# Kernel tuning notes

Hardware: AMD Instinct MI355X
Metric: run time of the kernel (lower is better)

## Reference

```python
import jax, jax.numpy as jnp
import numpy as np

B, TIN, E, TOUT, NMEL = 32, 512, 576, 400, 80
PRE, ARNN, DRNN, ADIM, NF, KS = 256, 1024, 1024, 128, 32, 31


def setup_inputs() -> dict:
    key = jax.random.key(0)
    ks = jax.random.split(key, 24)
    r = lambda i, sh, s=0.02: jax.random.normal(ks[i], sh, dtype=jnp.float32) * s
    return {
        'memory': jax.random.normal(ks[0], (B, TIN, E), dtype=jnp.float32) * 0.5,
        'decoder_inputs': jax.random.normal(ks[1], (B, TOUT, NMEL), dtype=jnp.float32) * 0.5,
        'prenet_W1': r(2, (PRE, NMEL)),
        'prenet_W2': r(3, (PRE, PRE)),
        'att_Wih': r(4, (4 * ARNN, PRE + E)),
        'att_Whh': r(5, (4 * ARNN, ARNN)),
        'att_bih': r(6, (4 * ARNN,)),
        'att_bhh': r(7, (4 * ARNN,)),
        'qW': r(8, (ADIM, ARNN)),
        'memW': r(9, (ADIM, E)),
        'convW': r(10, (NF, 2, KS)),
        'convb': r(11, (NF,)),
        'locW': r(12, (ADIM, NF)),
        'vW': r(13, (ADIM,)),
        'dec_Wih': r(14, (4 * DRNN, ARNN + E)),
        'dec_Whh': r(15, (4 * DRNN, DRNN)),
        'dec_bih': r(16, (4 * DRNN,)),
        'dec_bhh': r(17, (4 * DRNN,)),
        'projW': r(18, (NMEL, DRNN + E)),
        'projb': r(19, (NMEL,)),
        'gateW': r(20, (1, DRNN + E)),
        'gateb': r(21, (1,)),
        'memory_lengths': jnp.clip(jax.random.randint(ks[22], (B,), 1, TIN + 1), 16, TIN),
    }


def _lstm(x, h, c, Wih, Whh, bih, bhh):
    g = x @ Wih.T + bih + h @ Whh.T + bhh
    i, f, gg, o = jnp.split(g, 4, axis=-1)  # torch LSTMCell gate order i,f,g,o
    c = jax.nn.sigmoid(f) * c + jax.nn.sigmoid(i) * jnp.tanh(gg)
    h = jax.nn.sigmoid(o) * jnp.tanh(c)
    return h, c


def _forward(memory, decoder_inputs, prenet_W1, prenet_W2, att_Wih, att_Whh, att_bih,
             att_bhh, qW, memW, convW, convb, locW, vW, dec_Wih, dec_Whh, dec_bih,
             dec_bhh, projW, projb, gateW, gateb, memory_lengths):
    b, tin, e = memory.shape
    # go frame + teacher forcing inputs -> prenet (dropout off in deterministic eval)
    go = jnp.zeros((b, 1, NMEL), dtype=memory.dtype)
    di = jnp.concatenate([go, decoder_inputs], axis=1)          # [B, T+1, NMEL]
    x = jax.nn.relu(di @ prenet_W1.T)
    x = jax.nn.relu(x @ prenet_W2.T)                            # [B, T+1, PRE]
    xs = jnp.swapaxes(x, 0, 1)[:-1]                             # [T, B, PRE]
    pmem = memory @ memW.T                                      # [B, TIN, ADIM]
    invalid = jnp.arange(tin)[None, :] >= memory_lengths[:, None]
    pad = KS // 2

    init = (jnp.zeros((b, ARNN)), jnp.zeros((b, ARNN)),
            jnp.zeros((b, DRNN)), jnp.zeros((b, DRNN)),
            jnp.zeros((b, tin)), jnp.zeros((b, tin)),
            jnp.zeros((b, e)))

    def step(carry, xt):
        ah, ac, dh, dc, aw, awc, ctx = carry
        ci = jnp.concatenate([xt, ctx], axis=-1)
        ah, ac = _lstm(ci, ah, ac, att_Wih, att_Whh, att_bih, att_bhh)
        ah = ac  # faithful to source: dropout(attention_cell) overwrites hidden (identity in eval)
        wc = jnp.stack([aw, awc], axis=1)                       # [B, 2, TIN]
        loc = jax.lax.conv_general_dilated(
            wc, convW, (1,), [(pad, pad)],
            dimension_numbers=('NCH', 'OIH', 'NCH')) + convb[None, :, None]
        loc = jnp.swapaxes(loc, 1, 2) @ locW.T                  # [B, TIN, ADIM]
        q = (ah @ qW.T)[:, None, :]                             # [B, 1, ADIM]
        en = jnp.tanh(q + pmem + loc) @ vW                      # [B, TIN]
        en = jnp.where(invalid, -jnp.inf, en)
        aw = jax.nn.softmax(en, axis=1)
        ctx = jnp.einsum('bt,bte->be', aw, memory)
        awc = awc + aw
        d_in = jnp.concatenate([ah, ctx], axis=-1)
        dh, dc = _lstm(d_in, dh, dc, dec_Wih, dec_Whh, dec_bih, dec_bhh)
        dhc = jnp.concatenate([dh, ctx], axis=-1)
        mel = dhc @ projW.T + projb                             # [B, NMEL]
        gate = (dhc @ gateW.T + gateb)[:, 0]                    # [B]
        return (ah, ac, dh, dc, aw, awc, ctx), (mel, gate, aw)

    _, (mels, gates, aligns) = jax.lax.scan(step, init, xs)
    mel_out = jnp.swapaxes(jnp.swapaxes(mels, 0, 1), 1, 2)      # [B, NMEL, T]
    gate_out = jnp.swapaxes(gates, 0, 1)                        # [B, T]
    align_out = jnp.swapaxes(aligns, 0, 1)                      # [B, T, TIN]
    return mel_out, gate_out, align_out


def reference(memory, decoder_inputs, prenet_W1, prenet_W2, att_Wih, att_Whh, att_bih,
              att_bhh, qW, memW, convW, convb, locW, vW, dec_Wih, dec_Whh, dec_bih,
              dec_bhh, projW, projb, gateW, gateb, memory_lengths):
    return _forward(memory, decoder_inputs, prenet_W1, prenet_W2, att_Wih, att_Whh,
                    att_bih, att_bhh, qW, memW, convW, convb, locW, vW, dec_Wih,
                    dec_Whh, dec_bih, dec_bhh, projW, projb, gateW, gateb,
                    memory_lengths)
```

## Files before the change

### kernel.cpp

```cpp
#include <hip/hip_runtime.h>
#include <stdint.h>


#define NB  32
#define TI  512
#define ED  576
#define TO  400
#define NM  80
#define PR  256
#define AR  1024
#define DR  1024
#define AD  128
#define NFl 32
#define KSz 31
#define KA  1856
#define KD  2624
#define NKT_A 58
#define NKT_D 82
#define FPAD 32
#define MF_OFF (257*FPAD)

#define SCR_CWB 3584
#define SCR_ACC 4608
#define SCR_DCC 4736
#define SCR_SQ  4864
#define LDS_WA_BYTES (NKT_A*512*2)
#define LDS_WD_BYTES (NKT_D*512*2)
#define LDS_SCR_FLOATS 4992
#define LDS_TOTAL (LDS_WA_BYTES + LDS_WD_BYTES + LDS_SCR_FLOATS*4)

typedef __attribute__((ext_vector_type(8))) short bf8_t;
typedef __attribute__((ext_vector_type(4))) float f4_t;
typedef __attribute__((ext_vector_type(2))) float f2_t;
typedef unsigned long long ull;

__device__ __forceinline__ short f2bf(float f){
  union { float f; unsigned u; } v; v.f = f;
  unsigned r = v.u + 0x7fffu + ((v.u >> 16) & 1u);
  return (short)(r >> 16);
}
__device__ __forceinline__ float bf2f(short s){
  union { unsigned u; float f; } v; v.u = ((unsigned)(unsigned short)s) << 16; return v.f;
}
__device__ __forceinline__ float sigm(float x){ return 1.f / (1.f + __expf(-x)); }

__device__ __forceinline__ f4_t MFMA(bf8_t a, bf8_t b, f4_t c){
  return __builtin_amdgcn_mfma_f32_16x16x32_bf16(a, b, c, 0, 0, 0);
}

__device__ __forceinline__ float cld(const float* p){
  return __hip_atomic_load(p, __ATOMIC_RELAXED, __HIP_MEMORY_SCOPE_AGENT);
}
__device__ __forceinline__ void cst(float* p, float v){
  __hip_atomic_store(p, v, __ATOMIC_RELAXED, __HIP_MEMORY_SCOPE_AGENT);
}
__device__ __forceinline__ ull cld8(const void* p){
  return __hip_atomic_load((const ull*)p, __ATOMIC_RELAXED, __HIP_MEMORY_SCOPE_AGENT);
}
__device__ __forceinline__ void cst8(void* p, ull v){
  __hip_atomic_store((ull*)p, v, __ATOMIC_RELAXED, __HIP_MEMORY_SCOPE_AGENT);
}
__device__ __forceinline__ bf8_t cld_bf8(const short* p){
  union { bf8_t v; ull q[2]; } u;
  u.q[0] = cld8(p); u.q[1] = cld8(p + 4);
  return u.v;
}
__device__ __forceinline__ void cst_bf8(short* p, bf8_t v){
  union { bf8_t v; ull q[2]; } u; u.v = v;
  cst8(p, u.q[0]); cst8(p + 4, u.q[1]);
}

__device__ __forceinline__ bf8_t packrow(const float* p){
  f4_t a = *(const f4_t*)p;
  f4_t b = *(const f4_t*)(p + 4);
  bf8_t r;
  r[0]=f2bf(a[0]); r[1]=f2bf(a[1]); r[2]=f2bf(a[2]); r[3]=f2bf(a[3]);
  r[4]=f2bf(b[0]); r[5]=f2bf(b[1]); r[6]=f2bf(b[2]); r[7]=f2bf(b[3]);
  return r;
}
__device__ __forceinline__ bf8_t packrow_coh(const float* p){
  union { ull q; float f[2]; } u0, u1, u2, u3;
  u0.q = cld8(p); u1.q = cld8(p + 2); u2.q = cld8(p + 4); u3.q = cld8(p + 6);
  bf8_t r;
  r[0]=f2bf(u0.f[0]); r[1]=f2bf(u0.f[1]);
  r[2]=f2bf(u1.f[0]); r[3]=f2bf(u1.f[1]);
  r[4]=f2bf(u2.f[0]); r[5]=f2bf(u2.f[1]);
  r[6]=f2bf(u3.f[0]); r[7]=f2bf(u3.f[1]);
  return r;
}

struct Par {
  const float *X2;
  const short *PMEMH;
  const short *WA, *WD, *WQ, *WLOC, *MEMBT, *PJW;
  const float *BSA, *BSD;
  const float *convW, *convb, *vW;
  const float *projb, *gateb;
  const int *mlen;
  float *AC, *DH, *CTX, *AW, *AWC, *EN, *QP;
  short *ABA, *ABD;
  float *out_mel, *out_gate, *out_align;
  unsigned *FLAGS;
};

__device__ __forceinline__ const float* aptr_att(const Par& p, int rp, int t, int b, int k){
  if (k < PR)      return p.X2 + ((size_t)t*NB + b)*PR + k;
  if (k < PR+ED)   return p.CTX + (size_t)rp*NB*ED + b*ED + (k - PR);
  return p.AC + (size_t)b*AR + (k - PR - ED);
}

__device__ __forceinline__ void loadD(const Par& p, int cpar, int ks, int lane,
                                      bf8_t& a0, bf8_t& a1){
  if (ks >= 32 && ks < 50){
    const int kb = ks*32 + ((lane >> 4) << 3);
    const float* c0 = p.CTX + (size_t)cpar*NB*ED + (size_t)(lane & 15)*ED + (kb - AR);
    const float* c1 = p.CTX + (size_t)cpar*NB*ED + (size_t)(16 + (lane & 15))*ED + (kb - AR);
    a0 = packrow_coh(c0);
    a1 = packrow_coh(c1);
  } else {
    a0 = cld_bf8(p.ABD + ((size_t)(0*NKT_D + ks)*64 + lane)*8);
    a1 = cld_bf8(p.ABD + ((size_t)(1*NKT_D + ks)*64 + lane)*8);
  }
}

__device__ __forceinline__ void gbar(unsigned* flags, unsigned tgt){
  __syncthreads();
  if (threadIdx.x == 0)
    __hip_atomic_store(&flags[blockIdx.x*FPAD], tgt, __ATOMIC_RELAXED, __HIP_MEMORY_SCOPE_AGENT);
  if (blockIdx.x == 0){
    if (threadIdx.x < 256){
      while (__hip_atomic_load(&flags[threadIdx.x*FPAD], __ATOMIC_RELAXED, __HIP_MEMORY_SCOPE_AGENT) < tgt) {}
    }
    __syncthreads();
    if (threadIdx.x == 0)
      __hip_atomic_store(&flags[256*FPAD], tgt, __ATOMIC_RELAXED, __HIP_MEMORY_SCOPE_AGENT);
  }
  if (threadIdx.x == 0){
    while (__hip_atomic_load(&flags[256*FPAD], __ATOMIC_RELAXED, __HIP_MEMORY_SCOPE_AGENT) < tgt) {}
  }
  __syncthreads();
}

__device__ __forceinline__ void sibbar(unsigned* mf, int bid, int tid, unsigned tgt){
  __syncthreads();
  if (tid == 0)
    __hip_atomic_store(&mf[bid*FPAD], tgt, __ATOMIC_RELAXED, __HIP_MEMORY_SCOPE_AGENT);
  const int g = (bid >> 3) << 3;
  if (tid < 8){
    while (__hip_atomic_load(&mf[(g + tid)*FPAD], __ATOMIC_RELAXED, __HIP_MEMORY_SCOPE_AGENT) < tgt) {}
  }
  __syncthreads();
}

__device__ __forceinline__ void reduce8(float* scr, f4_t& a0, f4_t& a1, int lane, int wv){
  if (wv > 0){
    float* slot = scr + (size_t)((wv - 1)*64 + lane)*8;
    *(f4_t*)slot       = a0;
    *(f4_t*)(slot + 4) = a1;
  }
  __syncthreads();
  if (wv == 0){
    #pragma unroll
    for (int w = 0; w < 7; ++w){
      const float* s2 = scr + (size_t)(w*64 + lane)*8;
      a0 += *(const f4_t*)s2;
      a1 += *(const f4_t*)(s2 + 4);
    }
  }
  __syncthreads();
}

__device__ __forceinline__ void dec_gates_cell(const Par& p, const short* sWD, float* scr,
                                               float* sDCc, int cpar, int bid,
                                               int lane, int wv, int tid){
  f4_t acc0 = (f4_t){0.f,0.f,0.f,0.f}, acc1 = (f4_t){0.f,0.f,0.f,0.f};
  {
    bf8_t A0[6], A1[6];
    #pragma unroll
    for (int i = 0; i < 6; ++i) loadD(p, cpar, wv + i*8, lane, A0[i], A1[i]);
    #pragma unroll
    for (int i = 0; i < 6; ++i){
      const bf8_t bw = *((const bf8_t*)sWD + (wv + i*8)*64 + lane);
      acc0 = MFMA(A0[i], bw, acc0);
      acc1 = MFMA(A1[i], bw, acc1);
    }
  }
  {
    bf8_t A0[5], A1[5];
    #pragma unroll
    for (int i = 0; i < 5; ++i){
      const int ks = wv + (i + 6)*8;
      if (ks < NKT_D) loadD(p, cpar, ks, lane, A0[i], A1[i]);
    }
    #pragma unroll
    for (int i = 0; i < 5; ++i){
      const int ks = wv + (i + 6)*8;
      if (ks < NKT_D){
        const bf8_t bw = *((const bf8_t*)sWD + ks*64 + lane);
        acc0 = MFMA(A0[i], bw, acc0);
        acc1 = MFMA(A1[i], bw, acc1);
      }
    }
  }
  reduce8(scr, acc0, acc1, lane, wv);
  float* sG = scr;
  if (wv == 0){
    const int col = lane & 15, rb2 = (lane >> 4) << 2;
    const int jp = (col & 3)*1024 + bid*4 + (col >> 2);
    const float bs = p.BSD[jp];
    #pragma unroll
    for (int r = 0; r < 4; ++r){
      sG[(rb2 + r)*16 + col]      = acc0[r] + bs;
      sG[(16 + rb2 + r)*16 + col] = acc1[r] + bs;
    }
  }
  __syncthreads();
  if (tid < 128){
    const int b = tid >> 2, ul = tid & 3;
    const float gi = sG[b*16 + ul*4 + 0];
    const float gf = sG[b*16 + ul*4 + 1];
    const float gg = sG[b*16 + ul*4 + 2];
    const float go = sG[b*16 + ul*4 + 3];
    const float c  = sigm(gf) * sDCc[tid] + sigm(gi) * tanhf(gg);
    sDCc[tid] = c;
    cst(&p.DH[(size_t)b*DR + bid*4 + ul], sigm(go) * tanhf(c));
  }
  __syncthreads();
}

__device__ void dec_proj(const Par& p, int b, int tprev, int tid, float* sIN){
  const float* ctxg = p.CTX + (size_t)(tprev & 1)*NB*ED + b*ED;
  float h0  = cld(&p.DH[(size_t)b*DR + tid]);
  float h1  = cld(&p.DH[(size_t)b*DR + 512 + tid]);
  float cx0 = cld(ctxg + tid);
  float cx1 = (tid < ED - 512) ? cld(ctxg + 512 + tid) : 0.f;
  sIN[tid] = h0; sIN[512 + tid] = h1;
  sIN[1024 + tid] = cx0;
  if (tid < ED - 512) sIN[1536 + tid] = cx1;
  if (tid < 448) sIN[1600 + tid] = 0.f;
  __syncthreads();
  const int lane = tid & 63, wv = tid >> 6;
  for (int o = wv; o < 81; o += 8){
    const short* wr = p.PJW + (size_t)o*2048 + lane*8;
    float s = 0.f;
    #pragma unroll
    for (int j = 0; j < 4; ++j){
      const bf8_t w8 = *(const bf8_t*)(wr + j*512);
      const float* v = sIN + j*512 + lane*8;
      s += v[0]*bf2f(w8[0]) + v[1]*bf2f(w8[1]) + v[2]*bf2f(w8[2]) + v[3]*bf2f(w8[3])
         + v[4]*bf2f(w8[4]) + v[5]*bf2f(w8[5]) + v[6]*bf2f(w8[6]) + v[7]*bf2f(w8[7]);
    }
    #pragma unroll
    for (int d = 32; d > 0; d >>= 1) s += __shfl_down(s, d);
    if (lane == 0){
      if (o < 80) p.out_mel[((size_t)b*NM + o)*TO + tprev] = s + p.projb[o];
      else        p.out_gate[(size_t)b*TO + tprev] = s + p.gateb[0];
    }
  }
  __syncthreads();
}

__global__ __launch_bounds__(512) void k_loop(Par p){
  const int bid = blockIdx.x, tid = threadIdx.x;
  const int lane = tid & 63, wv = tid >> 6;

  extern __shared__ char dsm[];
  short* sWA = (short*)dsm;
  short* sWD = (short*)(dsm + LDS_WA_BYTES);
  float* scr = (float*)(dsm + LDS_WA_BYTES + LDS_WD_BYTES);
  float* sACc = scr + SCR_ACC;
  float* sDCc = scr + SCR_DCC;
  unsigned* mf = p.FLAGS + MF_OFF;

  const int mlenb = p.mlen[bid >> 3];

  {
    if (tid < 128){ sACc[tid] = 0.f; sDCc[tid] = 0.f; }
    const bf8_t* gwa = (const bf8_t*)(p.WA + (size_t)bid*NKT_A*512);
    bf8_t* lwa = (bf8_t*)sWA;
    for (int i = tid; i < NKT_A*64; i += 512) lwa[i] = gwa[i];
    const bf8_t* gwd = (const bf8_t*)(p.WD + (size_t)bid*NKT_D*512);
    bf8_t* lwd = (bf8_t*)sWD;
    for (int i = tid; i < NKT_D*64; i += 512) lwd[i] = gwd[i];
    __syncthreads();
  }

  for (int t = 0; t < TO; ++t){
    const int wp = t & 1, rp = wp ^ 1;
    const unsigned base = (unsigned)(t * 3);

    {
      f4_t acc0 = (f4_t){0.f,0.f,0.f,0.f}, acc1 = (f4_t){0.f,0.f,0.f,0.f};
      bf8_t A0[8], A1[8];
      #pragma unroll
      for (int i = 0; i < 8; ++i){
        const int ks = wv + i*8;
        if (ks < NKT_A){
          if (t == 0 || (ks >= 8 && ks < 26)){
            const int kb = ks*32 + ((lane >> 4) << 3);
            const float* p0 = aptr_att(p, rp, t, lane & 15, kb);
            const float* p1 = aptr_att(p, rp, t, 16 + (lane & 15), kb);
            if (kb < PR){ A0[i] = packrow(p0);     A1[i] = packrow(p1);     }
            else        { A0[i] = packrow_coh(p0); A1[i] = packrow_coh(p1); }
          } else {
            A0[i] = cld_bf8(p.ABA + ((size_t)(0*NKT_A + ks)*64 + lane)*8);
            A1[i] = cld_bf8(p.ABA + ((size_t)(1*NKT_A + ks)*64 + lane)*8);
          }
        }
      }
      #pragma unroll
      for (int i = 0; i < 8; ++i){
        const int ks = wv + i*8;
        if (ks < NKT_A){
          const bf8_t bw = *((const bf8_t*)sWA + ks*64 + lane);
          acc0 = MFMA(A0[i], bw, acc0);
          acc1 = MFMA(A1[i], bw, acc1);
        }
      }
      reduce8(scr, acc0, acc1, lane, wv);
      float* sG = scr;
      if (wv == 0){
        const int col = lane & 15, rb2 = (lane >> 4) << 2;
        const int jp = (col & 3)*1024 + bid*4 + (col >> 2);
        const float bs = p.BSA[jp];
        #pragma unroll
        for (int r = 0; r < 4; ++r){
          sG[(rb2 + r)*16 + col]      = acc0[r] + bs;
          sG[(16 + rb2 + r)*16 + col] = acc1[r] + bs;
        }
      }
      __syncthreads();
      if (tid < 128){
        const int b = tid >> 2, ul = tid & 3;
        const float gi = sG[b*16 + ul*4 + 0];
        const float gf = sG[b*16 + ul*4 + 1];
        const float gg = sG[b*16 + ul*4 + 2];
        const float c  = sigm(gf) * sACc[tid] + sigm(gi) * tanhf(gg);
        sACc[tid] = c;
        cst(&p.AC[(size_t)b*AR + bid*4 + ul], c);
      }
      __syncthreads();
      if (t > 0) dec_gates_cell(p, sWD, scr, sDCc, rp, bid, lane, wv, tid);
      const int b = bid >> 3, tc = bid & 7, t0 = tc*64;
      float* sAWI = scr;
      short* sCwB = (short*)(scr + SCR_CWB);
      for (int i = tid; i < 94; i += 512){
        int g = t0 - 15 + i;
        float a = 0.f, w = 0.f;
        if (g >= 0 && g < TI){
          a = cld(&p.AW [(size_t)rp*NB*TI + b*TI + g]);
          w = cld(&p.AWC[(size_t)rp*NB*TI + b*TI + g]);
        }
        sAWI[2*i] = a; sAWI[2*i + 1] = w;
      }
      __syncthreads();
      {
        const int wvu = __builtin_amdgcn_readfirstlane(wv);
        const int f0 = wvu * 4;
        float ac4[4];
        #pragma unroll
        for (int ff = 0; ff < 4; ++ff) ac4[ff] = p.convb[f0 + ff];
        for (int k = 0; k < KSz; ++k){
          f2_t a2 = *(const f2_t*)&sAWI[2*(lane + k)];
          #pragma unroll
          for (int ff = 0; ff < 4; ++ff){
            ac4[ff] += a2[0] * p.convW[((f0+ff)*2 + 0)*KSz + k]
                     + a2[1] * p.convW[((f0+ff)*2 + 1)*KSz + k];
          }
        }
        #pragma unroll
        for (int ff = 0; ff < 4; ++ff) sCwB[lane*32 + f0 + ff] = f2bf(ac4[ff]);
      }
    }
    gbar(p.FLAGS, base + 1);

    {
      if (bid < 32){
        const int nt = bid >> 2, kc = bid & 3;
        const int kt = kc*8 + wv;
        const int kb = kt*32 + ((lane >> 4) << 3);
        bf8_t a0 = packrow_coh(p.AC + (size_t)(lane & 15)*AR + kb);
        bf8_t a1 = packrow_coh(p.AC + (size_t)(16 + (lane & 15))*AR + kb);
        const bf8_t bw = *(const bf8_t*)(p.WQ + ((size_t)(nt*32 + kt)*64 + lane)*8);
        f4_t q0 = (f4_t){0.f,0.f,0.f,0.f}, q1 = (f4_t){0.f,0.f,0.f,0.f};
        q0 = MFMA(a0, bw, q0);
        q1 = MFMA(a1, bw, q1);
        reduce8(scr, q0, q1, lane, wv);
        if (wv == 0){
          const int col = lane & 15, rb2 = (lane >> 4) << 2;
          float* qp = p.QP + (size_t)kc*NB*AD;
          #pragma unroll
          for (int r = 0; r < 4; ++r){
            cst(&qp[(rb2 + r)*AD + nt*16 + col],      q0[r]);
            cst(&qp[(16 + rb2 + r)*AD + nt*16 + col], q1[r]);
          }
        }
      }
      if (bid >= 224 && t > 0) dec_proj(p, bid - 224, t - 1, tid, scr);
    }
    gbar(p.FLAGS, base + 2);

    {
      float* sQ = scr + SCR_SQ;
      if (tid < 128){
        const int b = bid >> 3;
        sQ[tid] = cld(&p.QP[(size_t)b*AD + tid])
                + cld(&p.QP[(size_t)NB*AD + b*AD + tid])
                + cld(&p.QP[(size_t)2*NB*AD + b*AD + tid])
                + cld(&p.QP[(size_t)3*NB*AD + b*AD + tid]);
      }
      if (wv == 0 && bid < 208){
        const int r = lane & 15, koff = (lane >> 4) << 3;
        if (bid < 80){
          if (t < TO - 1){
            const int m = bid / 40, idx = bid % 40;
            const int ks = (idx < 8) ? idx : idx + 18;
            const int row = m*16 + r;
            const int k = ks*32 + koff;
            bf8_t v = (k < PR)
              ? packrow(p.X2 + ((size_t)(t+1)*NB + row)*PR + k)
              : packrow_coh(p.AC + (size_t)row*AR + (k - PR - ED));
            cst_bf8(p.ABA + ((size_t)(m*NKT_A + ks)*64 + lane)*8, v);
          }
        } else {
          const int j2 = bid - 80;
          const int m = j2 / 64, idx = j2 % 64;
          const int ks = (idx < 32) ? idx : idx + 18;
          const int row = m*16 + r;
          const int k = ks*32 + koff;
          bf8_t v = (k < AR)
            ? packrow_coh(p.AC + (size_t)row*AR + k)
            : packrow_coh(p.DH + (size_t)row*DR + (k - AR - ED));
          cst_bf8(p.ABD + ((size_t)(m*NKT_D + ks)*64 + lane)*8, v);
        }
      }
      __syncthreads();
      const int b = bid >> 3, tc = bid & 7, t0 = tc*64;
      short* sCwB = (short*)(scr + SCR_CWB);
      float* eP = scr;
      const int g = lane >> 4, li = lane & 15;
      const int d2 = wv*16 + li;
      const float vw = p.vW[d2];
      const float qd = sQ[d2];
      const bf8_t bfr = *(const bf8_t*)(p.WLOC + (size_t)(wv*64 + lane)*8);
      float pm[16];
      #pragma unroll
      for (int mt = 0; mt < 4; ++mt){
        #pragma unroll
        for (int r = 0; r < 4; ++r)
          pm[mt*4 + r] = bf2f(p.PMEMH[((size_t)b*TI + t0 + mt*16 + g*4 + r)*AD + d2]);
      }
      #pragma unroll
      for (int mt = 0; mt < 4; ++mt){
        const bf8_t afr = *(const bf8_t*)(sCwB + (mt*16 + li)*32 + (g << 3));
        f4_t c = (f4_t){0.f,0.f,0.f,0.f};
        c = MFMA(afr, bfr, c);
        #pragma unroll
        for (int r = 0; r < 4; ++r){
          const float val = c[r] + pm[mt*4 + r];
          float v = vw * tanhf(qd + val);
          v += __shfl_xor(v, 1);
          v += __shfl_xor(v, 2);
          v += __shfl_xor(v, 4);
          v += __shfl_xor(v, 8);
          if (li == 0) eP[wv*64 + mt*16 + g*4 + r] = v;
        }
      }
      __syncthreads();
      if (tid < 64){
        float e = eP[tid];
        #pragma unroll
        for (int w2 = 1; w2 < 8; ++w2) e += eP[w2*64 + tid];
        const int tg = t0 + tid;
        cst(&p.EN[b*TI + tg], (tg < mlenb) ? e : -1e30f);
      }
    }
    sibbar(mf, bid, tid, (unsigned)(t + 1));

    {
      const int b = bid >> 3, ec = bid & 7;
      float* red = scr;
      float* sp  = scr + 64;
      const float e = cld(&p.EN[b*TI + tid]);
      float m = e;
      #pragma unroll
      for (int d = 32; d > 0; d >>= 1) m = fmaxf(m, __shfl_xor(m, d));
      if (lane == 0) red[wv] = m;
      __syncthreads();
      const float M = fmaxf(fmaxf(fmaxf(red[0], red[1]), fmaxf(red[2], red[3])),
                            fmaxf(fmaxf(red[4], red[5]), fmaxf(red[6], red[7])));
      const float x = __expf(e - M);
      float z = x;
      #pragma unroll
      for (int d = 32; d > 0; d >>= 1) z += __shfl_xor(z, d);
      __syncthreads();
      if (lane == 0) red[wv] = z;
      __syncthreads();
      const float Z = red[0]+red[1]+red[2]+red[3]+red[4]+red[5]+red[6]+red[7];
      const float pv = x / Z;
      sp[tid] = pv;
      __syncthreads();
      if (ec == 0){
        cst(&p.AW [(size_t)wp*NB*TI + b*TI + tid], pv);
        cst(&p.AWC[(size_t)wp*NB*TI + b*TI + tid],
            cld(&p.AWC[(size_t)rp*NB*TI + b*TI + tid]) + pv);
        p.out_align[((size_t)b*TO + t)*TI + tid] = pv;
      }
      const float* vp = sp + lane*8;
      const float v0 = vp[0], v1 = vp[1], v2 = vp[2], v3 = vp[3];
      const float v4 = vp[4], v5 = vp[5], v6 = vp[6], v7 = vp[7];
      const bool act = (lane*8 < mlenb);
      #pragma unroll
      for (int ii = 0; ii < 9; ++ii){
        const int e2 = ec*72 + wv*9 + ii;
        float a2 = 0.f;
        if (act){
          const bf8_t w8 = *(const bf8_t*)(p.MEMBT + ((size_t)b*ED + e2)*TI + lane*8);
          a2 = v0*bf2f(w8[0]) + v1*bf2f(w8[1]) + v2*bf2f(w8[2]) + v3*bf2f(w8[3])
             + v4*bf2f(w8[4]) + v5*bf2f(w8[5]) + v6*bf2f(w8[6]) + v7*bf2f(w8[7]);
        }
        #pragma unroll
        for (int d = 32; d > 0; d >>= 1) a2 += __shfl_down(a2, d);
        if (lane == 0)
          cst(&p.CTX[(size_t)wp*NB*ED + b*ED + e2], a2);
      }
    }
    gbar(p.FLAGS, base + 3);
  }

  dec_gates_cell(p, sWD, scr, sDCc, (TO - 1) & 1, bid, lane, wv, tid);
  gbar(p.FLAGS, (unsigned)(TO*3 + 1));
  if (bid >= 224) dec_proj(p, bid - 224, TO - 1, tid, scr);
}

__global__ __launch_bounds__(256) void k_init(float* z, int nz,
                                              float* bsa, const float* a1, const float* a2,
                                              float* bsd, const float* d1, const float* d2){
  const int idx = blockIdx.x*256 + threadIdx.x, st = gridDim.x*256;
  const int NG = 4096;
  for (int i = idx; i < nz; i += st) z[i] = 0.f;
  for (int i = idx; i < NG; i += st){ bsa[i] = a1[i] + a2[i]; bsd[i] = d1[i] + d2[i]; }
}

__global__ __launch_bounds__(256) void k_prenet1(const float* di, const float* W1, float* X1){
  const int t = blockIdx.x, tid = threadIdx.x;
  __shared__ float sdi[NB*NM];
  for (int i = tid; i < NB*NM; i += 256){
    const int b = i / NM, k = i - b*NM;
    sdi[i] = (t == 0) ? 0.f : di[((size_t)b*TO + (t-1))*NM + k];
  }
  __syncthreads();
  float acc[NB];
  #pragma unroll
  for (int b = 0; b < NB; ++b) acc[b] = 0.f;
  const int j = tid;
  for (int k = 0; k < NM; ++k){
    const float w = W1[j*NM + k];
    #pragma unroll
    for (int b = 0; b < NB; ++b) acc[b] += sdi[b*NM + k] * w;
  }
  for (int b = 0; b < NB; ++b)
    X1[((size_t)t*NB + b)*PR + j] = fmaxf(acc[b], 0.f);
}

__global__ __launch_bounds__(256) void k_prenet2(const float* X1, const float* W2, float* X2){
  const int t = blockIdx.x, tid = threadIdx.x;
  __shared__ float sx[NB*PR];
  for (int i = tid; i < NB*PR; i += 256) sx[i] = X1[(size_t)t*NB*PR + i];
  __syncthreads();
  float acc[NB];
  #pragma unroll
  for (int b = 0; b < NB; ++b) acc[b] = 0.f;
  const int j = tid;
  for (int k = 0; k < PR; ++k){
    const float w = W2[j*PR + k];
    #pragma unroll
    for (int b = 0; b < NB; ++b) acc[b] += sx[b*PR + k] * w;
  }
  for (int b = 0; b < NB; ++b)
    X2[((size_t)t*NB + b)*PR + j] = fmaxf(acc[b], 0.f);
}

__global__ __launch_bounds__(256) void k_pmem(const float* mem, const float* memW, short* pm){
  const int b = blockIdx.x >> 3, tc = blockIdx.x & 7, tid = threadIdx.x;
  __shared__ float sW[64*AD];
  __shared__ float sM[64*65];
  const int tl = tid >> 2, dq = tid & 3;
  float acc[32];
  #pragma unroll
  for (int i = 0; i < 32; ++i) acc[i] = 0.f;
  for (int kc = 0; kc < 9; ++kc){
    __syncthreads();
    for (int i = tid; i < 64*AD; i += 256){
      const int d = i >> 6, kl = i & 63;
      sW[kl*AD + ((d + kl) & 127)] = memW[(size_t)d*ED + kc*64 + kl];
    }
    for (int i = tid; i < 64*64; i += 256){
      const int tt = i >> 6, kl = i & 63;
      sM[tt*65 + kl] = mem[((size_t)b*TI + tc*64 + tt)*ED + kc*64 + kl];
    }
    __syncthreads();
    for (int kl = 0; kl < 64; ++kl){
      const float mv = sM[tl*65 + kl];
      #pragma unroll
      for (int d2 = 0; d2 < 32; ++d2)
        acc[d2] += mv * sW[kl*AD + ((dq*32 + d2 + kl) & 127)];
    }
  }
  for (int d2 = 0; d2 < 32; ++d2)
    pm[((size_t)b*TI + tc*64 + tl)*AD + dq*32 + d2] = f2bf(acc[d2]);
}

__global__ __launch_bounds__(256) void k_membt(const float* mem, short* mt){
  const int b = blockIdx.x / 36, ec = blockIdx.x % 36;
  __shared__ float sT[64*17];
  for (int tc = 0; tc < 8; ++tc){
    __syncthreads();
    for (int i = threadIdx.x; i < 64*16; i += 256){
      const int tt = i >> 4, e = i & 15;
      sT[tt*17 + e] = mem[((size_t)b*TI + tc*64 + tt)*ED + ec*16 + e];
    }
    __syncthreads();
    for (int i = threadIdx.x; i < 16*64; i += 256){
      const int e = i >> 6, tt = i & 63;
      mt[((size_t)b*ED + ec*16 + e)*TI + tc*64 + tt] = f2bf(sT[tt*17 + e]);
    }
  }
}

__global__ __launch_bounds__(64) void k_swz_gate(const float* Wih, const float* Whh,
                                                 short* dst, int split, int nkt){
  const int bidx = blockIdx.x;
  const int nt = bidx / nkt, kt = bidx - nt*nkt;
  const int lane = threadIdx.x;
  const int nl = lane & 15;
  const int jp = (nl & 3)*1024 + nt*4 + (nl >> 2);
  const int k0 = kt*32 + ((lane >> 4) << 3);
  bf8_t v;
  #pragma unroll
  for (int jj = 0; jj < 8; ++jj){
    const int k = k0 + jj;
    const float f = (k < split) ? Wih[(size_t)jp*split + k]
                                : Whh[(size_t)jp*1024 + (k - split)];
    v[jj] = f2bf(f);
  }
  *(bf8_t*)(dst + (size_t)bidx*512 + lane*8) = v;
}

__global__ __launch_bounds__(64) void k_swz_q(const float* qW, short* dst){
  const int bidx = blockIdx.x;
  const int nt = bidx >> 5, kt = bidx & 31;
  const int lane = threadIdx.x;
  const int d = nt*16 + (lane & 15);
  const int k0 = kt*32 + ((lane >> 4) << 3);
  bf8_t v;
  #pragma unroll
  for (int jj = 0; jj < 8; ++jj) v[jj] = f2bf(qW[(size_t)d*AR + k0 + jj]);
  *(bf8_t*)(dst + (size_t)bidx*512 + lane*8) = v;
}

__global__ __launch_bounds__(64) void k_swz_loc(const float* locW, short* dst){
  const int nt = blockIdx.x;
  const int lane = threadIdx.x;
  const int d = nt*16 + (lane & 15);
  const int f0 = (lane >> 4) << 3;
  bf8_t v;
  #pragma unroll
  for (int jj = 0; jj < 8; ++jj) v[jj] = f2bf(locW[d*NFl + f0 + jj]);
  *(bf8_t*)(dst + (size_t)(nt*64 + lane)*8) = v;
}

__global__ __launch_bounds__(256) void k_swz_proj(const float* projW, const float* gateW,
                                                  short* dst){
  const int o = blockIdx.x;
  const float* src = (o < 80) ? (projW + (size_t)o*1600) : gateW;
  for (int k = threadIdx.x; k < 2048; k += 256)
    dst[(size_t)o*2048 + k] = (k < 1600) ? f2bf(src[k]) : (short)0;
}

extern "C" void kernel_launch(void* const* d_in, const int* in_sizes, int n_in,
                              void* d_out, int out_size, void* d_ws, size_t ws_size,
                              hipStream_t stream){
  const float* mem    = (const float*)d_in[0];
  const float* dec_in = (const float*)d_in[1];
  const float* pW1    = (const float*)d_in[2];
  const float* pW2    = (const float*)d_in[3];
  const float* aWih   = (const float*)d_in[4];
  const float* aWhh   = (const float*)d_in[5];
  const float* aBih   = (const float*)d_in[6];
  const float* aBhh   = (const float*)d_in[7];
  const float* qW     = (const float*)d_in[8];
  const float* memW   = (const float*)d_in[9];
  const float* convW  = (const float*)d_in[10];
  const float* convb  = (const float*)d_in[11];
  const float* locW   = (const float*)d_in[12];
  const float* vW     = (const float*)d_in[13];
  const float* dWih   = (const float*)d_in[14];
  const float* dWhh   = (const float*)d_in[15];
  const float* dBih   = (const float*)d_in[16];
  const float* dBhh   = (const float*)d_in[17];
  const float* projW  = (const float*)d_in[18];
  const float* projb  = (const float*)d_in[19];
  const float* gateW  = (const float*)d_in[20];
  const float* gateb  = (const float*)d_in[21];
  const int*   mlen   = (const int*)d_in[22];
  (void)in_sizes; (void)n_in; (void)out_size; (void)ws_size;

  char* basep = (char*)d_ws;
  size_t off = 0;
  auto carve = [&](size_t bytes) -> char* {
    char* r = basep + off;
    off = (off + bytes + 255) & ~(size_t)255;
    return r;
  };
  const int NG = 4096;
  short* WA    = (short*)carve((size_t)NG*KA*2);
  short* WD    = (short*)carve((size_t)NG*KD*2);
  short* WQ    = (short*)carve((size_t)AD*AR*2);
  short* WLOC  = (short*)carve((size_t)AD*NFl*2);
  short* MEMBT = (short*)carve((size_t)NB*TI*ED*2);
  short* PJW   = (short*)carve((size_t)81*2048*2);
  short* PMEMH = (short*)carve((size_t)NB*TI*AD*2);
  float* X1    = (float*)carve((size_t)TO*NB*PR*4);
  float* X2    = (float*)carve((size_t)TO*NB*PR*4);
  float* BSA   = (float*)carve((size_t)NG*4);
  float* BSD   = (float*)carve((size_t)NG*4);
  short* ABA   = (short*)carve((size_t)2*NKT_A*512*2);
  short* ABD   = (short*)carve((size_t)2*NKT_D*512*2);
  float* AC    = (float*)carve((size_t)NB*AR*4);
  float* DH    = (float*)carve((size_t)NB*DR*4);
  float* CTX   = (float*)carve((size_t)2*NB*ED*4);
  float* AW    = (float*)carve((size_t)2*NB*TI*4);
  float* AWC   = (float*)carve((size_t)2*NB*TI*4);
  float* EN    = (float*)carve((size_t)NB*TI*4);
  float* QP    = (float*)carve((size_t)4*NB*AD*4);
  unsigned* FLAGS = (unsigned*)carve((size_t)(MF_OFF + 256*FPAD)*4);
  const int nz = (int)((((char*)FLAGS + (size_t)(MF_OFF + 256*FPAD)*4) - (char*)AC) / 4);

  float* out_mel   = (float*)d_out;
  float* out_gate  = out_mel + (size_t)NB*NM*TO;
  float* out_align = out_gate + (size_t)NB*TO;

  k_init   <<<dim3(512), dim3(256), 0, stream>>>(AC, nz, BSA, aBih, aBhh, BSD, dBih, dBhh);
  k_prenet1<<<dim3(TO),  dim3(256), 0, stream>>>(dec_in, pW1, X1);
  k_prenet2<<<dim3(TO),  dim3(256), 0, stream>>>(X1, pW2, X2);
  k_pmem   <<<dim3(256), dim3(256), 0, stream>>>(mem, memW, PMEMH);
  k_membt  <<<dim3(NB*36), dim3(256), 0, stream>>>(mem, MEMBT);
  k_swz_gate<<<dim3(256*NKT_A), dim3(64), 0, stream>>>(aWih, aWhh, WA, 832, NKT_A);
  k_swz_gate<<<dim3(256*NKT_D), dim3(64), 0, stream>>>(dWih, dWhh, WD, 1600, NKT_D);
  k_swz_q  <<<dim3(256), dim3(64), 0, stream>>>(qW, WQ);
  k_swz_loc<<<dim3(8),   dim3(64), 0, stream>>>(locW, WLOC);
  k_swz_proj<<<dim3(81), dim3(256), 0, stream>>>(projW, gateW, PJW);

  Par p;
  p.X2 = X2; p.PMEMH = PMEMH;
  p.WA = WA; p.WD = WD; p.WQ = WQ; p.WLOC = WLOC; p.MEMBT = MEMBT; p.PJW = PJW;
  p.BSA = BSA; p.BSD = BSD;
  p.convW = convW; p.convb = convb; p.vW = vW;
  p.projb = projb; p.gateb = gateb;
  p.mlen = mlen;
  p.AC = AC; p.DH = DH; p.CTX = CTX;
  p.AW = AW; p.AWC = AWC; p.EN = EN; p.QP = QP;
  p.ABA = ABA; p.ABD = ABD;
  p.out_mel = out_mel; p.out_gate = out_gate; p.out_align = out_align;
  p.FLAGS = FLAGS;

  (void)hipFuncSetAttribute((const void*)k_loop,
                            hipFuncAttributeMaxDynamicSharedMemorySize, LDS_TOTAL);
  k_loop<<<dim3(256), dim3(512), LDS_TOTAL, stream>>>(p);
}
```

Before: 30.71 ms.

## Compute query projection redundantly per block to drop one grid barrier per step

Each of the 8 blocks serving a batch row now computes the full 128-wide query projection for that row itself from the attention hidden state, using a transposed bf16 weight layout. Before, 32 blocks computed it with MFMA and wrote partial sums to global memory, which cost an extra grid-wide barrier every step. The mel/gate projection work is also spread across all 256 blocks (about 10 outputs each) instead of 32 blocks. This cuts three barriers per timestep to two, at the price of 8x redundant query FLOPs and weight reads per batch row on scalar FP32 math.

```diff
diff --git a/kernel.cpp b/kernel.cpp
--- a/kernel.cpp
+++ b/kernel.cpp
@@ -92,12 +92,12 @@
 struct Par {
   const float *X2;
   const short *PMEMH;
-  const short *WA, *WD, *WQ, *WLOC, *MEMBT, *PJW;
+  const short *WA, *WD, *QWP, *WLOC, *MEMBT, *PJW;
   const float *BSA, *BSD;
   const float *convW, *convb, *vW;
   const float *projb, *gateb;
   const int *mlen;
-  float *AC, *DH, *CTX, *AW, *AWC, *EN, *QP;
+  float *AC, *DH, *CTX, *AW, *AWC, *EN;
   short *ABA, *ABD;
   float *out_mel, *out_gate, *out_align;
   unsigned *FLAGS;
@@ -228,28 +228,16 @@
   __syncthreads();
 }
 
-__device__ void dec_proj(const Par& p, int b, int tprev, int tid, float* sIN){
-  const float* ctxg = p.CTX + (size_t)(tprev & 1)*NB*ED + b*ED;
-  float h0  = cld(&p.DH[(size_t)b*DR + tid]);
-  float h1  = cld(&p.DH[(size_t)b*DR + 512 + tid]);
-  float cx0 = cld(ctxg + tid);
-  float cx1 = (tid < ED - 512) ? cld(ctxg + 512 + tid) : 0.f;
-  sIN[tid] = h0; sIN[512 + tid] = h1;
-  sIN[1024 + tid] = cx0;
-  if (tid < ED - 512) sIN[1536 + tid] = cx1;
-  if (tid < 448) sIN[1600 + tid] = 0.f;
-  __syncthreads();
-  const int lane = tid & 63, wv = tid >> 6;
-  for (int o = wv; o < 81; o += 8){
-    const short* wr = p.PJW + (size_t)o*2048 + lane*8;
+__device__ __forceinline__ void proj_do(const Par& p, int b, int r8, int tprev,
+                                        int lane, int wv, const float* sIN2){
+  const int no = (r8 == 7) ? 11 : 10, o0 = r8*10;
+  for (int oi = wv; oi < no; oi += 8){
+    const int o = o0 + oi;
+    const short* wr = p.PJW + (size_t)o*2048;
     float s = 0.f;
     #pragma unroll
-    for (int j = 0; j < 4; ++j){
-      const bf8_t w8 = *(const bf8_t*)(wr + j*512);
-      const float* v = sIN + j*512 + lane*8;
-      s += v[0]*bf2f(w8[0]) + v[1]*bf2f(w8[1]) + v[2]*bf2f(w8[2]) + v[3]*bf2f(w8[3])
-         + v[4]*bf2f(w8[4]) + v[5]*bf2f(w8[5]) + v[6]*bf2f(w8[6]) + v[7]*bf2f(w8[7]);
-    }
+    for (int i2 = 0; i2 < 25; ++i2)
+      s += sIN2[lane + 64*i2] * bf2f(wr[lane + 64*i2]);
     #pragma unroll
     for (int d = 32; d > 0; d >>= 1) s += __shfl_down(s, d);
     if (lane == 0){
@@ -257,7 +245,6 @@
       else        p.out_gate[(size_t)b*TO + tprev] = s + p.gateb[0];
     }
   }
-  __syncthreads();
 }
 
 __global__ __launch_bounds__(512) void k_loop(Par p){
@@ -287,7 +274,7 @@
 
   for (int t = 0; t < TO; ++t){
     const int wp = t & 1, rp = wp ^ 1;
-    const unsigned base = (unsigned)(t * 3);
+    const unsigned base = (unsigned)(t * 2);
 
     {
       f4_t acc0 = (f4_t){0.f,0.f,0.f,0.f}, acc1 = (f4_t){0.f,0.f,0.f,0.f};
@@ -375,39 +362,39 @@
     gbar(p.FLAGS, base + 1);
 
     {
-      if (bid < 32){
-        const int nt = bid >> 2, kc = bid & 3;
-        const int kt = kc*8 + wv;
-        const int kb = kt*32 + ((lane >> 4) << 3);
-        bf8_t a0 = packrow_coh(p.AC + (size_t)(lane & 15)*AR + kb);
-        bf8_t a1 = packrow_coh(p.AC + (size_t)(16 + (lane & 15))*AR + kb);
-        const bf8_t bw = *(const bf8_t*)(p.WQ + ((size_t)(nt*32 + kt)*64 + lane)*8);
-        f4_t q0 = (f4_t){0.f,0.f,0.f,0.f}, q1 = (f4_t){0.f,0.f,0.f,0.f};
-        q0 = MFMA(a0, bw, q0);
-        q1 = MFMA(a1, bw, q1);
-        reduce8(scr, q0, q1, lane, wv);
-        if (wv == 0){
-          const int col = lane & 15, rb2 = (lane >> 4) << 2;
-          float* qp = p.QP + (size_t)kc*NB*AD;
-          #pragma unroll
-          for (int r = 0; r < 4; ++r){
-            cst(&qp[(rb2 + r)*AD + nt*16 + col],      q0[r]);
-            cst(&qp[(16 + rb2 + r)*AD + nt*16 + col], q1[r]);
-          }
-        }
-      }
-      if (bid >= 224 && t > 0) dec_proj(p, bid - 224, t - 1, tid, scr);
-    }
-    gbar(p.FLAGS, base + 2);
-
-    {
-      float* sQ = scr + SCR_SQ;
-      if (tid < 128){
-        const int b = bid >> 3;
-        sQ[tid] = cld(&p.QP[(size_t)b*AD + tid])
-                + cld(&p.QP[(size_t)NB*AD + b*AD + tid])
-                + cld(&p.QP[(size_t)2*NB*AD + b*AD + tid])
-                + cld(&p.QP[(size_t)3*NB*AD + b*AD + tid]);
+      const int b = bid >> 3, tc = bid & 7, t0 = tc*64;
+      float* sACrow = scr;
+      float* sIN2   = scr + 1024;
+      float* sQ     = scr + SCR_SQ;
+      const float ac0 = cld(&p.AC[(size_t)b*AR + tid]);
+      const float ac1 = cld(&p.AC[(size_t)b*AR + 512 + tid]);
+      float dh0 = 0.f, dh1 = 0.f, cx0 = 0.f, cx1 = 0.f;
+      if (t > 0){
+        dh0 = cld(&p.DH[(size_t)b*DR + tid]);
+        dh1 = cld(&p.DH[(size_t)b*DR + 512 + tid]);
+        const float* ctxg = p.CTX + (size_t)rp*NB*ED + b*ED;
+        cx0 = cld(ctxg + tid);
+        if (tid < 64) cx1 = cld(ctxg + 512 + tid);
+      }
+      sACrow[tid] = ac0; sACrow[512 + tid] = ac1;
+      sIN2[tid] = dh0; sIN2[512 + tid] = dh1;
+      sIN2[1024 + tid] = cx0;
+      if (tid < 64) sIN2[1536 + tid] = cx1;
+      __syncthreads();
+      {
+        const int d = wv*16 + (lane & 15), qq = lane >> 4;
+        float acc = 0.f;
+        const short* qwp = p.QWP + (size_t)qq*32*1024 + d*8;
+        #pragma unroll
+        for (int i = 0; i < 32; ++i){
+          const bf8_t w8 = *(const bf8_t*)(qwp + i*1024);
+          const float* av = sACrow + qq*256 + i*8;
+          acc += av[0]*bf2f(w8[0]) + av[1]*bf2f(w8[1]) + av[2]*bf2f(w8[2]) + av[3]*bf2f(w8[3])
+               + av[4]*bf2f(w8[4]) + av[5]*bf2f(w8[5]) + av[6]*bf2f(w8[6]) + av[7]*bf2f(w8[7]);
+        }
+        acc += __shfl_down(acc, 32);
+        acc += __shfl_down(acc, 16);
+        if (lane < 16) sQ[wv*16 + lane] = acc;
       }
       if (wv == 0 && bid < 208){
         const int r = lane & 15, koff = (lane >> 4) << 3;
@@ -435,7 +422,7 @@
         }
       }
       __syncthreads();
-      const int b = bid >> 3, tc = bid & 7, t0 = tc*64;
+      if (t > 0) proj_do(p, b, tc, t - 1, lane, wv, sIN2);
       short* sCwB = (short*)(scr + SCR_CWB);
       float* eP = scr;
       const int g = lane >> 4, li = lane & 15;
@@ -525,12 +512,22 @@
           cst(&p.CTX[(size_t)wp*NB*ED + b*ED + e2], a2);
       }
     }
-    gbar(p.FLAGS, base + 3);
+    gbar(p.FLAGS, base + 2);
   }
 
   dec_gates_cell(p, sWD, scr, sDCc, (TO - 1) & 1, bid, lane, wv, tid);
-  gbar(p.FLAGS, (unsigned)(TO*3 + 1));
-  if (bid >= 224) dec_proj(p, bid - 224, TO - 1, tid, scr);
+  gbar(p.FLAGS, (unsigned)(TO*2 + 1));
+  {
+    const int b = bid >> 3, r8 = bid & 7;
+    float* sIN2 = scr + 1024;
+    sIN2[tid]       = cld(&p.DH[(size_t)b*DR + tid]);
+    sIN2[512 + tid] = cld(&p.DH[(size_t)b*DR + 512 + tid]);
+    const float* ctxg = p.CTX + (size_t)((TO - 1) & 1)*NB*ED + b*ED;
+    sIN2[1024 + tid] = cld(ctxg + tid);
+    if (tid < 64) sIN2[1536 + tid] = cld(ctxg + 512 + tid);
+    __syncthreads();
+    proj_do(p, b, r8, TO - 1, lane, wv, sIN2);
+  }
 }
 
 __global__ __launch_bounds__(256) void k_init(float* z, int nz,
@@ -647,16 +644,12 @@
   *(bf8_t*)(dst + (size_t)bidx*512 + lane*8) = v;
 }
 
-__global__ __launch_bounds__(64) void k_swz_q(const float* qW, short* dst){
-  const int bidx = blockIdx.x;
-  const int nt = bidx >> 5, kt = bidx & 31;
-  const int lane = threadIdx.x;
-  const int d = nt*16 + (lane & 15);
-  const int k0 = kt*32 + ((lane >> 4) << 3);
-  bf8_t v;
+__global__ __launch_bounds__(128) void k_swz_qt(const float* qW, short* dst){
+  const int kb = blockIdx.x;
+  const int d  = threadIdx.x;
   #pragma unroll
-  for (int jj = 0; jj < 8; ++jj) v[jj] = f2bf(qW[(size_t)d*AR + k0 + jj]);
-  *(bf8_t*)(dst + (size_t)bidx*512 + lane*8) = v;
+  for (int j = 0; j < 8; ++j)
+    dst[(size_t)kb*1024 + d*8 + j] = f2bf(qW[(size_t)d*AR + kb*8 + j]);
 }
 
 __global__ __launch_bounds__(64) void k_swz_loc(const float* locW, short* dst){
@@ -716,7 +709,7 @@
   const int NG = 4096;
   short* WA    = (short*)carve((size_t)NG*KA*2);
   short* WD    = (short*)carve((size_t)NG*KD*2);
-  short* WQ    = (short*)carve((size_t)AD*AR*2);
+  short* QWP   = (short*)carve((size_t)AD*AR*2);
   short* WLOC  = (short*)carve((size_t)AD*NFl*2);
   short* MEMBT = (short*)carve((size_t)NB*TI*ED*2);
   short* PJW   = (short*)carve((size_t)81*2048*2);
@@ -733,7 +726,6 @@
   float* AW    = (float*)carve((size_t)2*NB*TI*4);
   float* AWC   = (float*)carve((size_t)2*NB*TI*4);
   float* EN    = (float*)carve((size_t)NB*TI*4);
-  float* QP    = (float*)carve((size_t)4*NB*AD*4);
   unsigned* FLAGS = (unsigned*)carve((size_t)(MF_OFF + 256*FPAD)*4);
   const int nz = (int)((((char*)FLAGS + (size_t)(MF_OFF + 256*FPAD)*4) - (char*)AC) / 4);
 
@@ -748,19 +740,19 @@
   k_membt  <<<dim3(NB*36), dim3(256), 0, stream>>>(mem, MEMBT);
   k_swz_gate<<<dim3(256*NKT_A), dim3(64), 0, stream>>>(aWih, aWhh, WA, 832, NKT_A);
   k_swz_gate<<<dim3(256*NKT_D), dim3(64), 0, stream>>>(dWih, dWhh, WD, 1600, NKT_D);
-  k_swz_q  <<<dim3(256), dim3(64), 0, stream>>>(qW, WQ);
+  k_swz_qt <<<dim3(128), dim3(128), 0, stream>>>(qW, QWP);
   k_swz_loc<<<dim3(8),   dim3(64), 0, stream>>>(locW, WLOC);
   k_swz_proj<<<dim3(81), dim3(256), 0, stream>>>(projW, gateW, PJW);
 
   Par p;
   p.X2 = X2; p.PMEMH = PMEMH;
-  p.WA = WA; p.WD = WD; p.WQ = WQ; p.WLOC = WLOC; p.MEMBT = MEMBT; p.PJW = PJW;
+  p.WA = WA; p.WD = WD; p.QWP = QWP; p.WLOC = WLOC; p.MEMBT = MEMBT; p.PJW = PJW;
   p.BSA = BSA; p.BSD = BSD;
   p.convW = convW; p.convb = convb; p.vW = vW;
   p.projb = projb; p.gateb = gateb;
   p.mlen = mlen;
   p.AC = AC; p.DH = DH; p.CTX = CTX;
-  p.AW = AW; p.AWC = AWC; p.EN = EN; p.QP = QP;
+  p.AW = AW; p.AWC = AWC; p.EN = EN;
   p.ABA = ABA; p.ABD = ABD;
   p.out_mel = out_mel; p.out_gate = out_gate; p.out_align = out_align;
   p.FLAGS = FLAGS;
```

After: 33.64 ms. +9.5%, slower.
